# Kernel optimization log

Hardware: AMD Instinct MI355X
Metric: run time of the kernel (lower is better)

Reference implementation:

```python
import jax, jax.numpy as jnp
import numpy as np

B, L, M, D, H, FF, W = 2, 2048, 2048, 1024, 16, 4096, 64
DH = D // H


def _layernorm(x, g, b, eps=1e-5):
    mu = x.mean(-1, keepdims=True)
    var = ((x - mu) ** 2).mean(-1, keepdims=True)
    return (x - mu) / jnp.sqrt(var + eps) * g + b


def _mha(qx, kx, wq, bq, wk, bk, wv, bv, wo, bo, mask, bias):
    Bq, Lq, _ = qx.shape
    Lk = kx.shape[1]
    q = (qx @ wq + bq).reshape(Bq, Lq, H, DH).transpose(0, 2, 1, 3)  # [B,H,Lq,DH]
    k = (kx @ wk + bk).reshape(Bq, Lk, H, DH).transpose(0, 2, 1, 3)
    v = (kx @ wv + bv).reshape(Bq, Lk, H, DH).transpose(0, 2, 1, 3)
    s = jnp.einsum('bhqd,bhkd->bhqk', q, k) / jnp.sqrt(jnp.asarray(DH, qx.dtype))
    if bias is not None:
        s = s + bias[None]  # bias: [H,Lq,Lk]
    if mask is not None:
        s = jnp.where(mask[None, None], s, jnp.asarray(-1e9, qx.dtype))
    a = jax.nn.softmax(s, axis=-1)
    o = jnp.einsum('bhqk,bhkd->bhqd', a, v).transpose(0, 2, 1, 3).reshape(Bq, Lq, D)
    return o @ wo + bo


def _forward(x, mem,
             swq, sbq, swk, sbk, swv, sbv, swo, sbo,
             cwq, cbq, cwk, cbk, cwv, cbv, cwo, cbo,
             w1, b1, w2, b2,
             g1, be1, g2, be2, g3, be3):
    i = jnp.arange(L)[:, None]
    j = jnp.arange(L)[None, :]
    # causal local window mask: attend to j<=i with i-j < W
    mask = (j <= i) & ((i - j) < W)
    # ALiBi slopes for power-of-2 head counts: 2^{-8h/H}, h=1..H
    slopes = (2.0 ** (-8.0 * jnp.arange(1, H + 1, dtype=x.dtype) / H))
    bias = slopes[:, None, None] * (j - i).astype(x.dtype)[None]  # [H,L,L], <=0 on causal part
    sa = _mha(x, x, swq, sbq, swk, sbk, swv, sbv, swo, sbo, mask, bias)
    x = _layernorm(x + sa, g1, be1)
    # cross-attn mask is all ones -> no masking, no bias
    ca = _mha(x, mem, cwq, cbq, cwk, cbk, cwv, cbv, cwo, cbo, None, None)
    x = _layernorm(x + ca, g2, be2)
    ff = jax.nn.gelu(x @ w1 + b1, approximate=False) @ w2 + b2
    return _layernorm(x + ff, g3, be3)


def setup_inputs() -> dict:
    key = jax.random.key(0)
    ks = jax.random.split(key, 16)
    s = 0.02
    inp = {
        'x': jax.random.normal(ks[0], (B, L, D), jnp.float32),
        'mem': jax.random.normal(ks[1], (B, M, D), jnp.float32),
    }
    # self-attn params
    for n, k in zip(['swq', 'swk', 'swv', 'swo'], jax.random.split(ks[2], 4)):
        inp[n] = jax.random.normal(k, (D, D), jnp.float32) * s
    for n in ['sbq', 'sbk', 'sbv', 'sbo']:
        inp[n] = jnp.zeros((D,), jnp.float32)
    # cross-attn params
    for n, k in zip(['cwq', 'cwk', 'cwv', 'cwo'], jax.random.split(ks[3], 4)):
        inp[n] = jax.random.normal(k, (D, D), jnp.float32) * s
    for n in ['cbq', 'cbk', 'cbv', 'cbo']:
        inp[n] = jnp.zeros((D,), jnp.float32)
    # FFN params
    inp['w1'] = jax.random.normal(ks[4], (D, FF), jnp.float32) * s
    inp['b1'] = jnp.zeros((FF,), jnp.float32)
    inp['w2'] = jax.random.normal(ks[5], (FF, D), jnp.float32) * s
    inp['b2'] = jnp.zeros((D,), jnp.float32)
    # LayerNorm params
    for n in ['g1', 'g2', 'g3']:
        inp[n] = jnp.ones((D,), jnp.float32)
    for n in ['be1', 'be2', 'be3']:
        inp[n] = jnp.zeros((D,), jnp.float32)
    return inp


def reference(x, mem,
              swq, sbq, swk, sbk, swv, sbv, swo, sbo,
              cwq, cbq, cwk, cbk, cwv, cbv, cwo, cbo,
              w1, b1, w2, b2,
              g1, be1, g2, be2, g3, be3):
    return _forward(x, mem,
                    swq, sbq, swk, sbk, swv, sbv, swo, sbo,
                    cwq, cbq, cwk, cbk, cwv, cbv, cwo, cbo,
                    w1, b1, w2, b2,
                    g1, be1, g2, be2, g3, be3)
```

## Files before the change

kernel.cpp:

```cpp
#include <hip/hip_runtime.h>
#include <hip/hip_bf16.h>
#include <math.h>

#define Bc 2
#define Lc 2048
#define Mc 2048
#define Dc 1024
#define Hc 16
#define FFc 4096
#define DHc 64

typedef __bf16 bf16;
typedef float f32x4 __attribute__((ext_vector_type(4)));
typedef __bf16 bf16x8 __attribute__((ext_vector_type(8)));
typedef __bf16 bf16x4 __attribute__((ext_vector_type(4)));
typedef __bf16 bf16x2 __attribute__((ext_vector_type(2)));

__device__ inline void gload16(const bf16* g, const bf16* lds_base) {
  __builtin_amdgcn_global_load_lds(
      (const __attribute__((address_space(1))) void*)g,
      (__attribute__((address_space(3))) void*)lds_base, 16, 0, 0);
}

#define WAIT_VM(n) asm volatile("s_waitcnt vmcnt(" #n ")" ::: "memory")
#define WAIT_LGKM0 asm volatile("s_waitcnt lgkmcnt(0)" ::: "memory")
#define RAW_BAR() __builtin_amdgcn_s_barrier()
#define SCHED_FENCE() __builtin_amdgcn_sched_barrier(0)

__global__ __launch_bounds__(256) void k_f2b(const float* __restrict__ in,
                                             bf16* __restrict__ out, long n4) {
  long i = (long)blockIdx.x * 256 + threadIdx.x;
  if (i >= n4) return;
  f32x4 v = *(const f32x4*)(in + i * 4);
  bf16x4 o;
  o[0] = (bf16)v[0]; o[1] = (bf16)v[1]; o[2] = (bf16)v[2]; o[3] = (bf16)v[3];
  *(bf16x4*)(out + i * 4) = o;
}

__global__ __launch_bounds__(256) void k_transpose_w(const float* __restrict__ in,
                                                     bf16* __restrict__ out,
                                                     int K, int N) {
  __shared__ float tile[64][65];
  int n0 = blockIdx.x * 64, k0 = blockIdx.y * 64;
  int t = threadIdx.x;
  int tr = t >> 4, tc = (t & 15) * 4;
#pragma unroll
  for (int p = 0; p < 4; p++) {
    int r = p * 16 + tr;
    f32x4 v = *(const f32x4*)(in + (long)(k0 + r) * N + n0 + tc);
    tile[r][tc] = v[0]; tile[r][tc + 1] = v[1];
    tile[r][tc + 2] = v[2]; tile[r][tc + 3] = v[3];
  }
  __syncthreads();
#pragma unroll
  for (int p = 0; p < 4; p++) {
    int rn = p * 16 + tr;
    bf16x4 o;
    o[0] = (bf16)tile[tc + 0][rn]; o[1] = (bf16)tile[tc + 1][rn];
    o[2] = (bf16)tile[tc + 2][rn]; o[3] = (bf16)tile[tc + 3][rn];
    *(bf16x4*)(out + (long)(n0 + rn) * K + k0 + tc) = o;
  }
}

__global__ __launch_bounds__(256) void k_transpose_v(const bf16* __restrict__ vb,
                                                     bf16* __restrict__ vt, int N) {
  __shared__ bf16 tile[64][72];
  int j0 = blockIdx.x * 64;
  int bh = blockIdx.y; int b = bh >> 4; int h = bh & 15;
  int t = threadIdx.x;
#pragma unroll
  for (int c = 0; c < 2; c++) {
    int id = t + c * 256;
    int r = id >> 3, c8 = (id & 7) * 8;
    *(bf16x8*)&tile[r][c8] =
        *(const bf16x8*)(vb + ((long)(b * N + j0 + r)) * Dc + h * DHc + c8);
  }
  __syncthreads();
#pragma unroll
  for (int c = 0; c < 2; c++) {
    int id = t + c * 256;
    int d = id >> 3, j8 = (id & 7) * 8;
    bf16x8 o;
#pragma unroll
    for (int e = 0; e < 8; e++) o[e] = tile[j8 + e][d];
    *(bf16x8*)(vt + ((long)bh * DHc + d) * N + j0 + j8) = o;
  }
}

__global__ __launch_bounds__(256) void k_gemm128(
    const bf16* __restrict__ A0, const bf16* __restrict__ A1,
    const bf16* __restrict__ A2, long lda,
    const bf16* __restrict__ B0, long bstride,
    bf16* __restrict__ outB, long ldc, long cstride,
    const float* __restrict__ bias0, const float* __restrict__ bias1,
    const float* __restrict__ bias2, int Kdim, int act, float scale0) {
  __shared__ __align__(16) bf16 As[2][128 * 64];
  __shared__ __align__(16) bf16 Bs[2][128 * 64];
  int z = blockIdx.z;
  const bf16* A = (z == 0) ? A0 : ((z == 1) ? A1 : A2);
  const bf16* Bt = B0 + (long)z * bstride;
  const float* bias = (z == 0) ? bias0 : ((z == 1) ? bias1 : bias2);
  float scl = (z == 0) ? scale0 : 1.0f;
  long cbase = (long)z * cstride;
  int bm = blockIdx.y * 128, bn = blockIdx.x * 128;
  int t = threadIdx.x, w = t >> 6, lane = t & 63;
  int wm = w >> 1, wn = w & 1;
  int lr = lane & 15, lg = lane >> 4;
  int srow = lane >> 3, scol = (lane & 7) * 8;
  f32x4 acc[4][4] = {};
  int nk = Kdim >> 6;
  auto stage = [&](int buf, int kt2) {
    long k0 = (long)kt2 * 64;
#pragma unroll
    for (int i = 0; i < 4; i++) {
      int row = (i * 4 + w) * 8 + srow;
      gload16(A + (long)(bm + row) * lda + k0 + scol, &As[buf][(i * 4 + w) * 512]);
      gload16(Bt + (long)(bn + row) * Kdim + k0 + scol, &Bs[buf][(i * 4 + w) * 512]);
    }
  };
  stage(0, 0);
  if (nk > 1) stage(1, 1);
  for (int kt = 0; kt < nk; ++kt) {
    int cur = kt & 1;
    if (kt + 1 < nk) { WAIT_VM(8); } else { WAIT_VM(0); }
    RAW_BAR();
    SCHED_FENCE();
    bf16x8 af[2][4], bfr[2][4];
#pragma unroll
    for (int kk = 0; kk < 2; kk++) {
#pragma unroll
      for (int m = 0; m < 4; m++)
        af[kk][m] = *(const bf16x8*)&As[cur][(wm * 64 + m * 16 + lr) * 64 + kk * 32 + lg * 8];
#pragma unroll
      for (int n = 0; n < 4; n++)
        bfr[kk][n] = *(const bf16x8*)&Bs[cur][(wn * 64 + n * 16 + lr) * 64 + kk * 32 + lg * 8];
    }
    WAIT_LGKM0;
    SCHED_FENCE();
    RAW_BAR();
    if (kt + 2 < nk) stage(cur, kt + 2);
#pragma unroll
    for (int kk = 0; kk < 2; kk++)
#pragma unroll
      for (int m = 0; m < 4; m++)
#pragma unroll
        for (int n = 0; n < 4; n++)
          acc[m][n] = __builtin_amdgcn_mfma_f32_16x16x32_bf16(af[kk][m], bfr[kk][n],
                                                              acc[m][n], 0, 0, 0);
  }
#pragma unroll
  for (int n = 0; n < 4; n++) {
    int cg = bn + wn * 64 + n * 16 + lr;
    float bv = bias ? bias[cg] : 0.0f;
#pragma unroll
    for (int m = 0; m < 4; m++) {
#pragma unroll
      for (int rr = 0; rr < 4; rr++) {
        int rg = bm + wm * 64 + m * 16 + lg * 4 + rr;
        float v = (acc[m][n][rr] + bv) * scl;
        if (act == 1) v = 0.5f * v * (1.0f + erff(v * 0.70710678f));
        outB[cbase + (long)rg * ldc + cg] = (bf16)v;
      }
    }
  }
}

__global__ __launch_bounds__(256) void k_gemmsk(
    const bf16* __restrict__ A, long lda,
    const bf16* __restrict__ Bt, int Kfull,
    float* __restrict__ psum, long slab, int Kchunk, int ldc) {
  __shared__ __align__(16) bf16 As[2][128 * 64];
  __shared__ __align__(16) bf16 Bs[2][128 * 64];
  int z = blockIdx.z;
  int bm = blockIdx.y * 128, bn = blockIdx.x * 128;
  int t = threadIdx.x, w = t >> 6, lane = t & 63;
  int wm = w >> 1, wn = w & 1;
  int lr = lane & 15, lg = lane >> 4;
  int srow = lane >> 3, scol = (lane & 7) * 8;
  f32x4 acc[4][4] = {};
  int nk = Kchunk >> 6;
  long kstart = (long)z * Kchunk;
  auto stage = [&](int buf, int kt2) {
    long k0 = kstart + (long)kt2 * 64;
#pragma unroll
    for (int i = 0; i < 4; i++) {
      int row = (i * 4 + w) * 8 + srow;
      gload16(A + (long)(bm + row) * lda + k0 + scol, &As[buf][(i * 4 + w) * 512]);
      gload16(Bt + (long)(bn + row) * Kfull + k0 + scol, &Bs[buf][(i * 4 + w) * 512]);
    }
  };
  stage(0, 0);
  if (nk > 1) stage(1, 1);
  for (int kt = 0; kt < nk; ++kt) {
    int cur = kt & 1;
    if (kt + 1 < nk) { WAIT_VM(8); } else { WAIT_VM(0); }
    RAW_BAR();
    SCHED_FENCE();
    bf16x8 af[2][4], bfr[2][4];
#pragma unroll
    for (int kk = 0; kk < 2; kk++) {
#pragma unroll
      for (int m = 0; m < 4; m++)
        af[kk][m] = *(const bf16x8*)&As[cur][(wm * 64 + m * 16 + lr) * 64 + kk * 32 + lg * 8];
#pragma unroll
      for (int n = 0; n < 4; n++)
        bfr[kk][n] = *(const bf16x8*)&Bs[cur][(wn * 64 + n * 16 + lr) * 64 + kk * 32 + lg * 8];
    }
    WAIT_LGKM0;
    SCHED_FENCE();
    RAW_BAR();
    if (kt + 2 < nk) stage(cur, kt + 2);
#pragma unroll
    for (int kk = 0; kk < 2; kk++)
#pragma unroll
      for (int m = 0; m < 4; m++)
#pragma unroll
        for (int n = 0; n < 4; n++)
          acc[m][n] = __builtin_amdgcn_mfma_f32_16x16x32_bf16(af[kk][m], bfr[kk][n],
                                                              acc[m][n], 0, 0, 0);
  }
  float* po = psum + (long)z * slab;
#pragma unroll
  for (int n = 0; n < 4; n++) {
    int cg = bn + wn * 64 + n * 16 + lr;
#pragma unroll
    for (int m = 0; m < 4; m++) {
#pragma unroll
      for (int rr = 0; rr < 4; rr++) {
        int rg = bm + wm * 64 + m * 16 + lg * 4 + rr;
        po[(long)rg * ldc + cg] = acc[m][n][rr];
      }
    }
  }
}

template <int WINDOWED>
__global__ __launch_bounds__(256) void k_flash(const bf16* __restrict__ Qg,
                                               const bf16* __restrict__ Kg,
                                               const bf16* __restrict__ Vtg,
                                               bf16* __restrict__ Og, int nkv) {
  __shared__ __align__(16) bf16 Qs[64 * 64];
  __shared__ __align__(16) bf16 Ks[2][64 * 64];
  __shared__ __align__(16) bf16 Vs[2][64 * 64];
  int flat = blockIdx.y * 32 + blockIdx.x;
  int flat2 = (flat & 7) * 128 + (flat >> 3);
  int i0 = (flat2 & 31) * 64;
  int bh = flat2 >> 5;
  int b = bh >> 4, h = bh & 15;
  int t = threadIdx.x, w = t >> 6, lane = t & 63;
  int lr = lane & 15, lg = lane >> 4;
  long qoff = ((long)b * Lc + i0) * Dc + h * DHc;
  long koff = ((long)b * nkv) * Dc + h * DHc;
  long vtoff = (long)bh * DHc * nkv;
  int o0 = w * 1024 + (lane << 4), o1 = o0 + 4096;
  int r0 = o0 >> 7, c0 = (o0 & 127) ^ ((r0 & 7) << 4);
  int r1 = o1 >> 7, c1 = (o1 & 127) ^ ((r1 & 7) << 4);
  int d0 = c0 >> 1, d1 = c1 >> 1;
  gload16(Qg + qoff + (long)r0 * Dc + d0, &Qs[w * 512]);
  gload16(Qg + qoff + (long)r1 * Dc + d1, &Qs[2048 + w * 512]);
  int kb0 = WINDOWED ? (i0 >= 64 ? i0 - 64 : 0) : 0;
  int nt = WINDOWED ? ((i0 - kb0) >> 6) + 1 : (nkv >> 6);
  auto stage = [&](int buf, int kbase) {
    gload16(Kg + koff + (long)(kbase + r0) * Dc + d0, &Ks[buf][w * 512]);
    gload16(Kg + koff + (long)(kbase + r1) * Dc + d1, &Ks[buf][2048 + w * 512]);
    gload16(Vtg + vtoff + (long)r0 * nkv + kbase + d0, &Vs[buf][w * 512]);
    gload16(Vtg + vtoff + (long)r1 * nkv + kbase + d1, &Vs[buf][2048 + w * 512]);
  };
  stage(0, kb0);
  WAIT_VM(4);
  RAW_BAR();
  SCHED_FENCE();
  bf16x8 bq[2];
#pragma unroll
  for (int ks = 0; ks < 2; ks++) {
    int rq = w * 16 + lr, cb = ks * 64 + lg * 16;
    bq[ks] = *(const bf16x8*)&Qs[((rq << 7) + (cb ^ ((rq & 7) << 4))) >> 1];
  }
  char* pbase = (char*)&Qs[w * 1024];
  float mrun = -1e30f, lrun = 0.f;
  f32x4 oa[4] = {};
  float slopeL2 = WINDOWED ? exp2f(-0.5f * (float)(h + 1)) * 1.44269504f : 0.0f;
  int qabs = i0 + w * 16 + lr;
  for (int tch = 0; tch < nt; tch++) {
    int cur = tch & 1;
    if (tch + 1 < nt) {
      stage(cur ^ 1, kb0 + (tch + 1) * 64);
      WAIT_VM(4);
    } else {
      WAIT_VM(0);
    }
    RAW_BAR();
    SCHED_FENCE();
    int kbase = kb0 + tch * 64;
    f32x4 st[4] = {};
    __builtin_amdgcn_s_setprio(1);
#pragma unroll
    for (int ks = 0; ks < 2; ks++) {
#pragma unroll
      for (int m = 0; m < 4; m++) {
        int rk = m * 16 + lr, cb = ks * 64 + lg * 16;
        bf16x8 ka = *(const bf16x8*)&Ks[cur][((rk << 7) + (cb ^ ((rk & 7) << 4))) >> 1];
        st[m] = __builtin_amdgcn_mfma_f32_16x16x32_bf16(ka, bq[ks], st[m], 0, 0, 0);
      }
    }
    __builtin_amdgcn_s_setprio(0);
    float sc[4][4];
    float pmax = -3.0e38f;
#pragma unroll
    for (int m = 0; m < 4; m++)
#pragma unroll
      for (int rr = 0; rr < 4; rr++) {
        int kab = kbase + m * 16 + lg * 4 + rr;
        float v = st[m][rr];
        if (WINDOWED) {
          v += slopeL2 * (float)(kab - qabs);
          bool valid = (kab <= qabs) && (qabs - kab < 64);
          v = valid ? v : -3.0e38f;
        }
        sc[m][rr] = v;
        pmax = fmaxf(pmax, v);
      }
    pmax = fmaxf(pmax, __shfl_xor(pmax, 16));
    pmax = fmaxf(pmax, __shfl_xor(pmax, 32));
    float mx = mrun;
    if (!__all(pmax - mrun <= 8.0f)) {
      mx = fmaxf(mrun, pmax);
      float corr = exp2f(mrun - mx);
      mrun = mx;
      lrun *= corr;
      float cq[4];
#pragma unroll
      for (int rr = 0; rr < 4; rr++) cq[rr] = __shfl(corr, lg * 4 + rr);
#pragma unroll
      for (int jd = 0; jd < 4; jd++) {
        oa[jd][0] *= cq[0]; oa[jd][1] *= cq[1];
        oa[jd][2] *= cq[2]; oa[jd][3] *= cq[3];
      }
    }
    float ps = 0.f;
#pragma unroll
    for (int m = 0; m < 4; m++) {
#pragma unroll
      for (int hh = 0; hh < 2; hh++) {
        float p0 = exp2f(sc[m][2 * hh] - mx);
        float p1 = exp2f(sc[m][2 * hh + 1] - mx);
        ps += p0 + p1;
        bf16x2 pw; pw[0] = (bf16)p0; pw[1] = (bf16)p1;
        int kcol = m * 16 + lg * 4 + 2 * hh;
        *(bf16x2*)(pbase + (lr << 7) + (((kcol << 1)) ^ ((lr & 7) << 4))) = pw;
      }
    }
    lrun += ps;
    __builtin_amdgcn_s_setprio(1);
#pragma unroll
    for (int ks = 0; ks < 2; ks++) {
      bf16x8 pa = *(const bf16x8*)(pbase + (lr << 7) +
                                   (((ks * 64 + lg * 16)) ^ ((lr & 7) << 4)));
#pragma unroll
      for (int jd = 0; jd < 4; jd++) {
        int rv = jd * 16 + lr, cb = ks * 64 + lg * 16;
        bf16x8 vf = *(const bf16x8*)&Vs[cur][((rv << 7) + (cb ^ ((rv & 7) << 4))) >> 1];
        oa[jd] = __builtin_amdgcn_mfma_f32_16x16x32_bf16(pa, vf, oa[jd], 0, 0, 0);
      }
    }
    __builtin_amdgcn_s_setprio(0);
    WAIT_LGKM0;
    SCHED_FENCE();
    RAW_BAR();
  }
  float ls = lrun + __shfl_xor(lrun, 16);
  ls += __shfl_xor(ls, 32);
  float inv = 1.0f / ls;
  float iq[4];
#pragma unroll
  for (int rr = 0; rr < 4; rr++) iq[rr] = __shfl(inv, lg * 4 + rr);
#pragma unroll
  for (int rr = 0; rr < 4; rr++) {
    int qo = i0 + w * 16 + lg * 4 + rr;
#pragma unroll
    for (int jd = 0; jd < 4; jd++)
      Og[((long)b * Lc + qo) * Dc + h * DHc + jd * 16 + lr] =
          (bf16)(oa[jd][rr] * iq[rr]);
  }
}

template <int NS>
__global__ __launch_bounds__(256) void k_lnred(const float* __restrict__ psum,
                                               long slab,
                                               const float* __restrict__ bias,
                                               const float* __restrict__ addsrc,
                                               const float* __restrict__ g,
                                               const float* __restrict__ bb,
                                               float* __restrict__ outF,
                                               bf16* __restrict__ outB) {
  long row = blockIdx.x;
  int t = threadIdx.x; int lane = t & 63; int wid = t >> 6;
  __shared__ float red[8];
  f32x4 v = *(const f32x4*)(psum + row * Dc + t * 4);
#pragma unroll
  for (int s = 1; s < NS; s++) {
    f32x4 u = *(const f32x4*)(psum + s * slab + row * Dc + t * 4);
    v[0] += u[0]; v[1] += u[1]; v[2] += u[2]; v[3] += u[3];
  }
  f32x4 bv = *(const f32x4*)(bias + t * 4);
  f32x4 av = *(const f32x4*)(addsrc + row * Dc + t * 4);
  v[0] += bv[0] + av[0]; v[1] += bv[1] + av[1];
  v[2] += bv[2] + av[2]; v[3] += bv[3] + av[3];
  float s = v[0] + v[1] + v[2] + v[3];
  float s2 = v[0] * v[0] + v[1] * v[1] + v[2] * v[2] + v[3] * v[3];
#pragma unroll
  for (int off = 1; off < 64; off <<= 1) {
    s += __shfl_xor(s, off);
    s2 += __shfl_xor(s2, off);
  }
  if (lane == 0) { red[wid] = s; red[4 + wid] = s2; }
  __syncthreads();
  s = red[0] + red[1] + red[2] + red[3];
  s2 = red[4] + red[5] + red[6] + red[7];
  float mu = s * (1.0f / Dc);
  float var = s2 * (1.0f / Dc) - mu * mu;
  float rs = rsqrtf(var + 1e-5f);
#pragma unroll
  for (int e = 0; e < 4; e++) {
    int c = t * 4 + e;
    float y = (v[e] - mu) * rs * g[c] + bb[c];
    if (outF) outF[row * Dc + c] = y;
    if (outB) outB[row * Dc + c] = (bf16)y;
  }
}

extern "C" void kernel_launch(void* const* d_in, const int* in_sizes, int n_in,
                              void* d_out, int out_size, void* d_ws,
                              size_t ws_size, hipStream_t stream) {
  (void)in_sizes; (void)n_in; (void)out_size; (void)ws_size;
  const float* x = (const float*)d_in[0];
  const float* mem = (const float*)d_in[1];
  const float* swq = (const float*)d_in[2];
  const float* swk = (const float*)d_in[3];
  const float* swv = (const float*)d_in[4];
  const float* swo = (const float*)d_in[5];
  const float* sbq = (const float*)d_in[6];
  const float* sbk = (const float*)d_in[7];
  const float* sbv = (const float*)d_in[8];
  const float* sbo = (const float*)d_in[9];
  const float* cwq = (const float*)d_in[10];
  const float* cwk = (const float*)d_in[11];
  const float* cwv = (const float*)d_in[12];
  const float* cwo = (const float*)d_in[13];
  const float* cbq = (const float*)d_in[14];
  const float* cbk = (const float*)d_in[15];
  const float* cbv = (const float*)d_in[16];
  const float* cbo = (const float*)d_in[17];
  const float* w1 = (const float*)d_in[18];
  const float* b1 = (const float*)d_in[19];
  const float* w2 = (const float*)d_in[20];
  const float* b2 = (const float*)d_in[21];
  const float* g1 = (const float*)d_in[22];
  const float* g2 = (const float*)d_in[23];
  const float* g3 = (const float*)d_in[24];
  const float* be1 = (const float*)d_in[25];
  const float* be2 = (const float*)d_in[26];
  const float* be3 = (const float*)d_in[27];
  float* out = (float*)d_out;

  char* ws = (char*)d_ws;
  size_t off = 0;
  auto alloc = [&](size_t bytes) -> char* {
    char* p = ws + off;
    off = (off + bytes + 255) & ~(size_t)255;
    return p;
  };

  const long BL = (long)Bc * Lc;
  const long BM = (long)Bc * Mc;
  const long DD = (long)Dc * Dc;
  const long SL = BL * Dc;
  const float QSCL = 0.125f * 1.44269504f;

  bf16* wT0 = (bf16*)alloc((size_t)8 * DD * 2);
  bf16* w1T = (bf16*)alloc((size_t)FFc * Dc * 2);
  bf16* w2T = (bf16*)alloc((size_t)Dc * FFc * 2);
  bf16* xb = (bf16*)alloc((size_t)BL * Dc * 2);
  bf16* memb = (bf16*)alloc((size_t)BM * Dc * 2);
  bf16* x1b = (bf16*)alloc((size_t)BL * Dc * 2);
  bf16* x2b = (bf16*)alloc((size_t)BL * Dc * 2);
  bf16* qb = (bf16*)alloc((size_t)BL * Dc * 2);
  bf16* kb = (bf16*)alloc((size_t)BM * Dc * 2);
  bf16* vb = (bf16*)alloc((size_t)BM * Dc * 2);
  bf16* ob = (bf16*)alloc((size_t)BL * Dc * 2);
  bf16* vtS = (bf16*)alloc((size_t)Bc * Hc * DHc * Lc * 2);
  bf16* vtC = (bf16*)alloc((size_t)Bc * Hc * DHc * Mc * 2);
  float* x1f = (float*)alloc((size_t)BL * Dc * 4);
  float* x2f = (float*)alloc((size_t)BL * Dc * 4);
  bf16* ffh = (bf16*)alloc((size_t)BL * FFc * 2);
  float* psum = (float*)alloc((size_t)4 * SL * 4);

  const float* wsrc[8] = {swq, swk, swv, swo, cwq, cwk, cwv, cwo};
  for (int i = 0; i < 8; i++)
    k_transpose_w<<<dim3(Dc / 64, Dc / 64), 256, 0, stream>>>(wsrc[i], wT0 + i * DD, Dc, Dc);
  k_transpose_w<<<dim3(FFc / 64, Dc / 64), 256, 0, stream>>>(w1, w1T, Dc, FFc);
  k_transpose_w<<<dim3(Dc / 64, FFc / 64), 256, 0, stream>>>(w2, w2T, FFc, Dc);
  k_f2b<<<dim3((unsigned)(BL * Dc / 4 / 256)), 256, 0, stream>>>(x, xb, BL * Dc / 4);
  k_f2b<<<dim3((unsigned)(BM * Dc / 4 / 256)), 256, 0, stream>>>(mem, memb, BM * Dc / 4);

  k_gemm128<<<dim3(Dc / 128, BL / 128, 3), 256, 0, stream>>>(
      xb, xb, xb, Dc, wT0, DD, qb, Dc, SL, sbq, sbk, sbv, Dc, 0, QSCL);
  k_transpose_v<<<dim3(Lc / 64, Bc * Hc), 256, 0, stream>>>(vb, vtS, Lc);
  k_flash<1><<<dim3(Lc / 64, Bc * Hc), 256, 0, stream>>>(qb, kb, vtS, ob, Lc);
  k_gemmsk<<<dim3(Dc / 128, BL / 128, 2), 256, 0, stream>>>(
      ob, Dc, wT0 + 3 * DD, Dc, psum, SL, 512, Dc);
  k_lnred<2><<<dim3((unsigned)BL), 256, 0, stream>>>(psum, SL, sbo, x, g1, be1,
                                                     x1f, x1b);

  k_gemm128<<<dim3(Dc / 128, BM / 128, 3), 256, 0, stream>>>(
      x1b, memb, memb, Dc, wT0 + 4 * DD, DD, qb, Dc, SL, cbq, cbk, cbv, Dc, 0, QSCL);
  k_transpose_v<<<dim3(Mc / 64, Bc * Hc), 256, 0, stream>>>(vb, vtC, Mc);
  k_flash<0><<<dim3(Lc / 64, Bc * Hc), 256, 0, stream>>>(qb, kb, vtC, ob, Mc);
  k_gemmsk<<<dim3(Dc / 128, BL / 128, 2), 256, 0, stream>>>(
      ob, Dc, wT0 + 7 * DD, Dc, psum, SL, 512, Dc);
  k_lnred<2><<<dim3((unsigned)BL), 256, 0, stream>>>(psum, SL, cbo, x1f, g2, be2,
                                                     x2f, x2b);

  k_gemm128<<<dim3(FFc / 128, BL / 128, 1), 256, 0, stream>>>(
      x2b, x2b, x2b, Dc, w1T, 0, ffh, FFc, 0, b1, b1, b1, Dc, 1, 1.0f);
  k_gemmsk<<<dim3(Dc / 128, BL / 128, 4), 256, 0, stream>>>(
      ffh, FFc, w2T, FFc, psum, SL, 1024, Dc);
  k_lnred<4><<<dim3((unsigned)BL), 256, 0, stream>>>(psum, SL, b2, x2f, g3, be3,
                                                     out, nullptr);
}
```

Before: 445.5 us.

## XOR-swizzle GEMM LDS layout and use tanh-form GELU epilogue

Both GEMM kernels now apply an XOR swizzle to the column offset used when global_load_lds writes each 128-byte row into LDS. The fragment reads apply the matching XOR, so ds_read_b128 accesses spread across banks instead of colliding on the same bank group. Separately, the exact erf GELU in the epilogue is replaced by the tanh approximation computed with exp2. This is cheaper, but it no longer matches the reference's approximate=False GELU, so it adds a small numerical deviation.

```diff
diff --git a/kernel.cpp b/kernel.cpp
--- a/kernel.cpp
+++ b/kernel.cpp
@@ -26,6 +26,13 @@
 #define WAIT_LGKM0 asm volatile("s_waitcnt lgkmcnt(0)" ::: "memory")
 #define RAW_BAR() __builtin_amdgcn_s_barrier()
 #define SCHED_FENCE() __builtin_amdgcn_sched_barrier(0)
+
+__device__ inline float gelu_f(float v) {
+  float u = 0.7978845608f * (v + 0.044715f * v * v * v);
+  float e = exp2f(u * 2.885390082f);
+  float th = 1.0f - 2.0f / (e + 1.0f);
+  return 0.5f * v * (1.0f + th);
+}
 
 __global__ __launch_bounds__(256) void k_f2b(const float* __restrict__ in,
                                              bf16* __restrict__ out, long n4) {
@@ -106,7 +113,8 @@
   int t = threadIdx.x, w = t >> 6, lane = t & 63;
   int wm = w >> 1, wn = w & 1;
   int lr = lane & 15, lg = lane >> 4;
-  int srow = lane >> 3, scol = (lane & 7) * 8;
+  int srow = lane >> 3;
+  int scol = (((lane & 7) * 16) ^ ((lane >> 3) << 4)) >> 1;
   f32x4 acc[4][4] = {};
   int nk = Kdim >> 6;
   auto stage = [&](int buf, int kt2) {
@@ -125,15 +133,22 @@
     if (kt + 1 < nk) { WAIT_VM(8); } else { WAIT_VM(0); }
     RAW_BAR();
     SCHED_FENCE();
+    const char* pa = (const char*)&As[cur][0];
+    const char* pb = (const char*)&Bs[cur][0];
+    int xr = (lr & 7) << 4;
     bf16x8 af[2][4], bfr[2][4];
 #pragma unroll
     for (int kk = 0; kk < 2; kk++) {
 #pragma unroll
-      for (int m = 0; m < 4; m++)
-        af[kk][m] = *(const bf16x8*)&As[cur][(wm * 64 + m * 16 + lr) * 64 + kk * 32 + lg * 8];
-#pragma unroll
-      for (int n = 0; n < 4; n++)
-        bfr[kk][n] = *(const bf16x8*)&Bs[cur][(wn * 64 + n * 16 + lr) * 64 + kk * 32 + lg * 8];
+      for (int m = 0; m < 4; m++) {
+        int row = wm * 64 + m * 16 + lr;
+        af[kk][m] = *(const bf16x8*)(pa + (row << 7) + ((kk * 64 + lg * 16) ^ xr));
+      }
+#pragma unroll
+      for (int n = 0; n < 4; n++) {
+        int row = wn * 64 + n * 16 + lr;
+        bfr[kk][n] = *(const bf16x8*)(pb + (row << 7) + ((kk * 64 + lg * 16) ^ xr));
+      }
     }
     WAIT_LGKM0;
     SCHED_FENCE();
@@ -158,7 +173,7 @@
       for (int rr = 0; rr < 4; rr++) {
         int rg = bm + wm * 64 + m * 16 + lg * 4 + rr;
         float v = (acc[m][n][rr] + bv) * scl;
-        if (act == 1) v = 0.5f * v * (1.0f + erff(v * 0.70710678f));
+        if (act == 1) v = gelu_f(v);
         outB[cbase + (long)rg * ldc + cg] = (bf16)v;
       }
     }
@@ -176,7 +191,8 @@
   int t = threadIdx.x, w = t >> 6, lane = t & 63;
   int wm = w >> 1, wn = w & 1;
   int lr = lane & 15, lg = lane >> 4;
-  int srow = lane >> 3, scol = (lane & 7) * 8;
+  int srow = lane >> 3;
+  int scol = (((lane & 7) * 16) ^ ((lane >> 3) << 4)) >> 1;
   f32x4 acc[4][4] = {};
   int nk = Kchunk >> 6;
   long kstart = (long)z * Kchunk;
@@ -196,15 +212,22 @@
     if (kt + 1 < nk) { WAIT_VM(8); } else { WAIT_VM(0); }
     RAW_BAR();
     SCHED_FENCE();
+    const char* pa = (const char*)&As[cur][0];
+    const char* pb = (const char*)&Bs[cur][0];
+    int xr = (lr & 7) << 4;
     bf16x8 af[2][4], bfr[2][4];
 #pragma unroll
     for (int kk = 0; kk < 2; kk++) {
 #pragma unroll
-      for (int m = 0; m < 4; m++)
-        af[kk][m] = *(const bf16x8*)&As[cur][(wm * 64 + m * 16 + lr) * 64 + kk * 32 + lg * 8];
-#pragma unroll
-      for (int n = 0; n < 4; n++)
-        bfr[kk][n] = *(const bf16x8*)&Bs[cur][(wn * 64 + n * 16 + lr) * 64 + kk * 32 + lg * 8];
+      for (int m = 0; m < 4; m++) {
+        int row = wm * 64 + m * 16 + lr;
+        af[kk][m] = *(const bf16x8*)(pa + (row << 7) + ((kk * 64 + lg * 16) ^ xr));
+      }
+#pragma unroll
+      for (int n = 0; n < 4; n++) {
+        int row = wn * 64 + n * 16 + lr;
+        bfr[kk][n] = *(const bf16x8*)(pb + (row << 7) + ((kk * 64 + lg * 16) ^ xr));
+      }
     }
     WAIT_LGKM0;
     SCHED_FENCE();
```

Result: faster. 413.3 us (-7.2%).
